# Kernel optimization log

Measured on AMD Instinct MI355X. Metric: run time of the kernel, lower is better.

The kernel has to match this reference:

```python
import jax, jax.numpy as jnp
import numpy as np

B, C, W = 32, 128, 4096          # batch, channel (= emb_dim = D), window/input_dim
HID = [2048, 1024, 512]          # encoder hidden dims (last dim transforms)
K, D = 512, 128                  # codebook: K = hidden_dims[-1], D = emb_dim
BETA = 0.25


def setup_inputs() -> dict:
    key = jax.random.key(0)
    ks = jax.random.split(key, 12)
    def lin(k, fan_in, fan_out):
        return jax.random.normal(k, (fan_in, fan_out), jnp.float32) * (1.0 / np.sqrt(fan_in))
    inp = {"x": jax.random.normal(ks[0], (B, C, W), jnp.float32)}
    edims = [W] + HID  # 4096 -> 2048 -> 1024 -> 512
    for i in range(3):
        inp[f"ew{i}"] = lin(ks[1 + i], edims[i], edims[i + 1])
        inp[f"eb{i}"] = jnp.zeros((edims[i + 1],), jnp.float32)
    inp["codebook"] = jax.random.uniform(ks[4], (K, D), jnp.float32, -1.0 / K, 1.0 / K)
    ddims = [512, 1024, 2048, 4096]  # decoder mirrors encoder
    for i in range(3):
        inp[f"dw{i}"] = lin(ks[5 + i], ddims[i], ddims[i + 1])
        inp[f"db{i}"] = jnp.zeros((ddims[i + 1],), jnp.float32)
    return inp


def reference(x, ew0, eb0, ew1, eb1, ew2, eb2, codebook, dw0, db0, dw1, db1, dw2, db2):
    # ---- encoder: LinearBlock = Linear + ReLU over last dim ----
    h = x
    for wgt, b in ((ew0, eb0), (ew1, eb1), (ew2, eb2)):
        h = jax.nn.relu(h @ wgt + b)            # [B, C, L] with L shrinking to 512

    # ---- VectorQuantizer1d ----
    lat = jnp.swapaxes(h, 1, 2)                 # [B, L, D]
    flat = lat.reshape(-1, D)                   # [B*L, D]
    # cdist^2 via expansion, then argmin -> nearest-codebook lookup
    dist = (jnp.sum(flat * flat, axis=1, keepdims=True)
            + jnp.sum(codebook * codebook, axis=1)
            - 2.0 * flat @ codebook.T)          # [B*L, K]
    inds = jnp.argmin(dist, axis=1)             # [B*L]
    q = codebook[inds].reshape(lat.shape)       # one-hot matmul == gather

    commit = jnp.mean((jax.lax.stop_gradient(q) - lat) ** 2)
    embed = jnp.mean((q - jax.lax.stop_gradient(lat)) ** 2)
    vq_loss = BETA * commit + embed

    q_st = lat + jax.lax.stop_gradient(q - lat)  # straight-through estimator
    z = jnp.swapaxes(q_st, 1, 2)                 # back to [B, D, L]

    # ---- decoder: Linear+ReLU blocks, last block has no activation ----
    for i, (wgt, b) in enumerate(((dw0, db0), (dw1, db1), (dw2, db2))):
        z = z @ wgt + b
        if i < 2:
            z = jax.nn.relu(z)
    return z, x, vq_loss
```

## Files before the change

### kernel.cpp

```cpp
#include <hip/hip_runtime.h>


typedef _Float16 f16;
typedef _Float16 f16x8 __attribute__((ext_vector_type(8)));
typedef _Float16 f16x4 __attribute__((ext_vector_type(4)));
typedef float    f32x4 __attribute__((ext_vector_type(4)));

typedef const unsigned int __attribute__((address_space(1)))* gp1_t;
typedef unsigned int __attribute__((address_space(3)))*       lp3_t;

__device__ __forceinline__ void gl_lds16(const void* g, void* l) {
  __builtin_amdgcn_global_load_lds((gp1_t)g, (lp3_t)l, 16, 0, 0);
}

#define BATCH 32
#define CDIM  128
#define WDIM  4096
#define LDIM  512
#define KCB   512
#define DCB   128

#define SX    128.0f
#define SW    256.0f
#define SA    256.0f
#define SCB   4096.0f
#define SQ    4096.0f

#define G8_BAR() do { asm volatile("" ::: "memory"); \
  __builtin_amdgcn_s_barrier(); asm volatile("" ::: "memory"); } while (0)
#define G8_LGKM0() do { asm volatile("s_waitcnt lgkmcnt(0)" ::: "memory"); \
  __builtin_amdgcn_sched_barrier(0); } while (0)
#define G8_PRIO1() __builtin_amdgcn_s_setprio(1)
#define G8_PRIO0() __builtin_amdgcn_s_setprio(0)


#define GS_STAGE(src, row0, kk, off) \
  _Pragma("unroll") \
  for (int j_ = 0; j_ < 2; ++j_) { \
    const int p_ = j_ * 8192 + tid * 16; \
    const int r_ = p_ >> 6; \
    const int c_ = (p_ >> 4) & 3; \
    gl_lds16((src) + (size_t)((row0) + r_) * K + (kk) + ((c_ ^ ((r_ >> 1) & 3)) << 3), \
             smem + (off) + p_); \
  }

#define GS_ST(tt, pb, SRC, row0, poff) do { \
  const int tc_ = (tt) < NTloc ? (tt) : NTloc - 1; \
  const int kk_ = (t0 + tc_) << 5; \
  GS_STAGE(SRC, row0, kk_, (pb) * 65536 + (poff)) } while (0)

#define GS_READ_A(pb, HL, half, dst) \
  _Pragma("unroll") \
  for (int m_ = 0; m_ < 4; ++m_) { \
    const int r_ = wr * 128 + ((half) * 4 + m_) * 16 + fr; \
    dst[m_] = *(const f16x8*)(smem + (pb) * 65536 + (HL) * 16384 + r_ * 64 + swz16); \
  }

#define GS_READ_B(pb, HL, brr) \
  _Pragma("unroll") \
  for (int n_ = 0; n_ < 4; ++n_) { \
    const int r_ = wc * 64 + n_ * 16 + fr; \
    brr[n_] = *(const f16x8*)(smem + (pb) * 65536 + 32768 + (HL) * 16384 + r_ * 64 + swz16); \
  }

#define GS_MFMA(aarr, half, brr) \
  _Pragma("unroll") \
  for (int m_ = 0; m_ < 4; ++m_) \
  _Pragma("unroll") \
  for (int n_ = 0; n_ < 4; ++n_) \
    acc[(half) * 4 + m_][n_] = __builtin_amdgcn_mfma_f32_16x16x32_f16( \
        aarr[m_], brr[n_], acc[(half) * 4 + m_][n_], 0, 0, 0);

__global__ __launch_bounds__(512, 2)
void vq_gemmS(const f16* __restrict__ Ah, const f16* __restrict__ Al,
              const f16* __restrict__ Bh, const f16* __restrict__ Bl,
              float* __restrict__ Co, int M, int N, int K, int NTloc)
{
  __shared__ __align__(16) char smem[131072];

  const int tid = threadIdx.x;
  const int lane = tid & 63;
  const int w = tid >> 6;
  const int wr = w >> 2, wc = w & 3;
  const int fr = lane & 15, hq = lane >> 4;
  const int swz16 = (hq ^ ((fr >> 1) & 3)) << 4;

  const int nbx = N / 256;
  const int cpx = (int)gridDim.x >> 3;
  const int swzb = ((int)blockIdx.x & 7) * cpx + ((int)blockIdx.x >> 3);
  const int bx = swzb % nbx, by = swzb / nbx;
  const int m0 = by * 256, n0 = bx * 256;
  const int t0 = (int)blockIdx.y * NTloc;

  f32x4 acc[8][4] = {};
  f16x8 ah0[4], ah1[4], al0[4], al1[4], bh[4], bl[4];

  GS_ST(0, 0, Bh, n0, 32768); GS_ST(0, 0, Bl, n0, 49152);
  GS_ST(0, 0, Ah, m0, 0);     GS_ST(0, 0, Al, m0, 16384);
  GS_ST(1, 1, Bh, n0, 32768); GS_ST(1, 1, Bl, n0, 49152);
  GS_ST(1, 1, Ah, m0, 0);     GS_ST(1, 1, Al, m0, 16384);

  int pb = 0;
  for (int t = 0; t < NTloc; ++t) {
    asm volatile("s_waitcnt vmcnt(8)" ::: "memory");
    G8_BAR();
    GS_READ_A(pb, 0, 0, ah0) GS_READ_B(pb, 0, bh)
    G8_BAR(); G8_LGKM0();
    G8_PRIO1(); GS_MFMA(ah0, 0, bh) G8_PRIO0();
    G8_BAR();
    GS_READ_A(pb, 1, 0, al0) GS_READ_B(pb, 1, bl)
    GS_ST(t + 2, pb, Bh, n0, 32768);
    G8_BAR(); G8_LGKM0();
    G8_PRIO1(); GS_MFMA(ah0, 0, bl) G8_PRIO0();
    G8_BAR();
    GS_READ_A(pb, 0, 1, ah1)
    GS_ST(t + 2, pb, Bl, n0, 49152);
    G8_BAR(); G8_LGKM0();
    G8_PRIO1(); GS_MFMA(al0, 0, bh) G8_PRIO0();
    G8_BAR();
    GS_READ_A(pb, 1, 1, al1)
    GS_ST(t + 2, pb, Ah, m0, 0);
    G8_BAR(); G8_LGKM0();
    G8_PRIO1(); GS_MFMA(ah1, 1, bh) G8_PRIO0();
    G8_BAR();
    GS_ST(t + 2, pb, Al, m0, 16384);
    G8_PRIO1(); GS_MFMA(ah1, 1, bl) GS_MFMA(al1, 1, bh) G8_PRIO0();
    pb ^= 1;
  }

  float* Pslab = Co + (size_t)blockIdx.y * M * N;
  const int r4 = hq * 4;
#pragma unroll
  for (int mi = 0; mi < 8; ++mi) {
#pragma unroll
    for (int ni = 0; ni < 4; ++ni) {
      const int col = n0 + wc * 64 + ni * 16 + fr;
#pragma unroll
      for (int j = 0; j < 4; ++j) {
        const int row = m0 + wr * 128 + mi * 16 + r4 + j;
        Pslab[(size_t)row * N + col] = acc[mi][ni][j];
      }
    }
  }
}


#define G8_SRC(t, As, Bs, kk) \
  const f16 *As, *Bs; int kk; \
  { int ts_ = (t) < NTloc ? (t) : NTloc - 1; int kg_ = (t0 + ts_) << 6; \
    if (SPLIT) { int sg_ = (kg_ >= 2 * K) ? 2 : ((kg_ >= K) ? 1 : 0); \
      kk = kg_ - sg_ * K; As = (sg_ == 2) ? Al : Ah; Bs = (sg_ == 1) ? Bl : Bh; } \
    else { As = Ah; Bs = Bh; kk = kg_; } }

#define G8_STAGE(src, row0, kk, off) \
  _Pragma("unroll") \
  for (int j_ = 0; j_ < 2; ++j_) { \
    const int p_ = j_ * 8192 + tid * 16; \
    const int r_ = p_ >> 7; \
    const int c_ = (p_ >> 4) & 7; \
    gl_lds16((src) + (size_t)((row0) + r_) * K + (kk) + ((c_ ^ (r_ & 7)) << 3), \
             smem + (off) + p_); \
  }

#define G8_STAGE_A(t, u) do { G8_SRC(t, As_, Bs_, kk_) \
  G8_STAGE(As_, m0 + (u) * 128, kk_, ((t) & 1) * ASZ + (u) * 16384) } while (0)
#define G8_STAGE_B(t, u) do { G8_SRC(t, As_, Bs_, kk_) \
  G8_STAGE(Bs_, n0 + (u) * 128, kk_, BBASE + ((t) & 1) * BSZ + (u) * 16384) } while (0)

#define G8_READ_A(buf, mh) \
  _Pragma("unroll") \
  for (int m_ = 0; m_ < MR2; ++m_) { \
    const int r_ = wr * (MR * 16) + ((mh) * MR2 + m_) * 16 + fr; \
    _Pragma("unroll") \
    for (int ks_ = 0; ks_ < 2; ++ks_) \
      ar[m_][ks_] = *(const f16x8*)(smem + (buf) * ASZ + r_ * 128 + \
                                    ((((ks_ << 2) + hq) ^ (r_ & 7)) << 4)); \
  }

#define G8_READ_B(buf, nh, br) \
  _Pragma("unroll") \
  for (int n_ = 0; n_ < 2; ++n_) { \
    const int r_ = wc * 64 + ((nh) * 2 + n_) * 16 + fr; \
    _Pragma("unroll") \
    for (int ks_ = 0; ks_ < 2; ++ks_) \
      br[n_][ks_] = *(const f16x8*)(smem + BBASE + (buf) * BSZ + r_ * 128 + \
                                    ((((ks_ << 2) + hq) ^ (r_ & 7)) << 4)); \
  }

#define G8_MFMA(mh, nh, br) \
  _Pragma("unroll") \
  for (int m_ = 0; m_ < MR2; ++m_) \
  _Pragma("unroll") \
  for (int n_ = 0; n_ < 2; ++n_) \
  _Pragma("unroll") \
  for (int ks_ = 0; ks_ < 2; ++ks_) \
    acc[(mh) * MR2 + m_][(nh) * 2 + n_] = __builtin_amdgcn_mfma_f32_16x16x32_f16( \
        ar[m_][ks_], br[n_][ks_], acc[(mh) * MR2 + m_][(nh) * 2 + n_], 0, 0, 0);

#define G8_VMGATE() do { \
  if constexpr (BUNITS == 2) asm volatile("s_waitcnt vmcnt(4)" ::: "memory"); \
  else                       asm volatile("s_waitcnt vmcnt(2)" ::: "memory"); } while (0)

template<int SPLIT, int EPI, int WM, int WN, int MR>
__global__ __launch_bounds__(512, 2)
void vq_gemm8(const f16* __restrict__ Ah, const f16* __restrict__ Al,
              const f16* __restrict__ Bh, const f16* __restrict__ Bl,
              const float* __restrict__ bias,
              void* __restrict__ Co, void* __restrict__ Co2,
              int M, int N, int K, int NTloc, float unscale, float outscale)
{
  constexpr int MR2 = MR / 2;
  constexpr int GBM = WM * MR * 16;
  constexpr int GBN = WN * 64;
  constexpr int BUNITS = GBN / 128;
  constexpr int ASZ = GBM * 128;
  constexpr int BSZ = GBN * 128;
  constexpr int BBASE = 2 * ASZ;
  constexpr int LDSZ = 2 * ASZ + 2 * BSZ;

  __shared__ __align__(16) char smem[LDSZ];

  const int tid = threadIdx.x;
  const int lane = tid & 63;
  const int w = tid >> 6;
  const int wr = w / WN, wc = w % WN;
  const int fr = lane & 15, hq = lane >> 4;

  const int nbx = N / GBN;
  const int cpx = (int)gridDim.x >> 3;
  const int swz = ((int)blockIdx.x & 7) * cpx + ((int)blockIdx.x >> 3);
  const int bx = swz % nbx, by = swz / nbx;
  const int m0 = by * GBM, n0 = bx * GBN;
  const int t0 = (int)blockIdx.y * NTloc;

  const int NI = NTloc >> 1;

  f32x4 acc[MR][4] = {};
  f16x8 ar[MR2][2], br0[2][2], br1[2][2];

  G8_STAGE_B(0, 0); if constexpr (BUNITS == 2) G8_STAGE_B(0, 1);
  G8_STAGE_A(0, 0); G8_STAGE_A(0, 1);
  G8_STAGE_B(1, 0); if constexpr (BUNITS == 2) G8_STAGE_B(1, 1);

  for (int i = 0; i < NI; ++i) {
    const int to = 2 * i + 1, te = 2 * i + 2, to2 = 2 * i + 3;
    if constexpr (BUNITS == 1) {
      G8_VMGATE(); G8_BAR();
      G8_READ_A(0, 0) G8_READ_B(0, 0, br0) G8_READ_B(0, 1, br1)
      G8_STAGE_A(to, 0); G8_STAGE_A(to, 1);
      G8_BAR(); G8_LGKM0();
      G8_PRIO1(); G8_MFMA(0, 0, br0) G8_MFMA(0, 1, br1) G8_PRIO0();
      G8_BAR();
      G8_READ_A(0, 1)
      G8_STAGE_B(te, 0);
      G8_BAR(); G8_LGKM0();
      G8_PRIO1(); G8_MFMA(1, 0, br0) G8_MFMA(1, 1, br1) G8_PRIO0();
      G8_VMGATE(); G8_BAR();
      G8_READ_A(1, 0) G8_READ_B(1, 0, br0) G8_READ_B(1, 1, br1)
      G8_STAGE_A(te, 0); G8_STAGE_A(te, 1);
      G8_BAR(); G8_LGKM0();
      G8_PRIO1(); G8_MFMA(0, 0, br0) G8_MFMA(0, 1, br1) G8_PRIO0();
      G8_BAR();
      G8_READ_A(1, 1)
      G8_STAGE_B(to2, 0);
      G8_BAR(); G8_LGKM0();
      G8_PRIO1(); G8_MFMA(1, 0, br0) G8_MFMA(1, 1, br1) G8_PRIO0();
    } else {
      G8_VMGATE(); G8_BAR();
      G8_READ_A(0, 0) G8_READ_B(0, 0, br0)
      G8_STAGE_A(to, 0);
      G8_BAR(); G8_LGKM0(); G8_PRIO1(); G8_MFMA(0, 0, br0) G8_PRIO0();
      G8_BAR();
      G8_READ_B(0, 1, br1)
      G8_STAGE_A(to, 1);
      G8_BAR(); G8_LGKM0(); G8_PRIO1(); G8_MFMA(0, 1, br1) G8_PRIO0();
      G8_BAR();
      G8_READ_A(0, 1)
      G8_STAGE_B(te, 0);
      G8_BAR(); G8_LGKM0(); G8_PRIO1(); G8_MFMA(1, 0, br0) G8_PRIO0();
      G8_BAR();
      G8_STAGE_B(te, 1);
      G8_BAR(); G8_PRIO1(); G8_MFMA(1, 1, br1) G8_PRIO0();
      G8_VMGATE(); G8_BAR();
      G8_READ_A(1, 0) G8_READ_B(1, 0, br0)
      G8_STAGE_A(te, 0);
      G8_BAR(); G8_LGKM0(); G8_PRIO1(); G8_MFMA(0, 0, br0) G8_PRIO0();
      G8_BAR();
      G8_READ_B(1, 1, br1)
      G8_STAGE_A(te, 1);
      G8_BAR(); G8_LGKM0(); G8_PRIO1(); G8_MFMA(0, 1, br1) G8_PRIO0();
      G8_BAR();
      G8_READ_A(1, 1)
      G8_STAGE_B(to2, 0);
      G8_BAR(); G8_LGKM0(); G8_PRIO1(); G8_MFMA(1, 0, br0) G8_PRIO0();
      G8_BAR();
      G8_STAGE_B(to2, 1);
      G8_BAR(); G8_PRIO1(); G8_MFMA(1, 1, br1) G8_PRIO0();
    }
  }

  const int r4 = hq * 4;
#pragma unroll
  for (int mi = 0; mi < MR; ++mi) {
#pragma unroll
    for (int ni = 0; ni < 4; ++ni) {
      const int col = n0 + wc * 64 + ni * 16 + fr;
      const float bv = (EPI == 0) ? 0.f : bias[col];
#pragma unroll
      for (int j = 0; j < 4; ++j) {
        const int row = m0 + wr * (MR * 16) + mi * 16 + r4 + j;
        const size_t idx = (size_t)row * N + col;
        float y = acc[mi][ni][j] * unscale;
        if (EPI != 0) y += bv;
        if (EPI == 1 || EPI == 2) y = fmaxf(y, 0.f);
        if (EPI == 0 || EPI == 3) ((float*)Co)[idx] = y;
        else {
          const float ys = y * outscale;
          const f16 hv = (f16)ys;
          ((f16*)Co)[idx] = hv;
          if (EPI == 1) ((f16*)Co2)[idx] = (f16)(ys - (float)hv);
        }
      }
    }
  }
}

template<int NS>
__global__ void vq_ksum(const float* __restrict__ P, const float* __restrict__ bias,
                        f16* __restrict__ Oh, f16* __restrict__ Ol,
                        int MN, int N, float unscale, float outscale)
{
  const int i4 = (blockIdx.x * 256 + threadIdx.x) * 4;
  if (i4 >= MN) return;
  float4 s = ((const float4*)P)[i4 >> 2];
#pragma unroll
  for (int sl = 1; sl < NS; ++sl) {
    const float4 v = ((const float4*)(P + (size_t)sl * MN))[i4 >> 2];
    s.x += v.x; s.y += v.y; s.z += v.z; s.w += v.w;
  }
  const int col = i4 % N;
  f16x4 h, l;
#pragma unroll
  for (int j = 0; j < 4; ++j) {
    float y = (&s.x)[j] * unscale + bias[col + j];
    y = fmaxf(y, 0.f) * outscale;
    const f16 hv = (f16)y;
    h[j] = hv;
    l[j] = (f16)(y - (float)hv);
  }
  *(f16x4*)&Oh[i4] = h;
  *(f16x4*)&Ol[i4] = l;
}

#define BM 128
#define BN 128
#define BK 32

template<int SPLIT, int EPI>
__global__ __launch_bounds__(256, 2)
void vq_gemm(const f16* __restrict__ Ah, const f16* __restrict__ Al,
             const f16* __restrict__ Bh, const f16* __restrict__ Bl,
             const float* __restrict__ bias,
             void* __restrict__ Co, void* __restrict__ Co2,
             int M, int N, int K, float unscale, float outscale)
{
  __shared__ __align__(16) f16 sAh[BM * BK];
  __shared__ __align__(16) f16 sBh[BN * BK];
  __shared__ __align__(16) f16 sAl[SPLIT ? BM * BK : 8];
  __shared__ __align__(16) f16 sBl[SPLIT ? BN * BK : 8];

  const int tid  = threadIdx.x;
  const int lane = tid & 63;
  const int w    = tid >> 6;
  const int nb   = N / BN;
  const int bx   = blockIdx.x % nb;
  const int by   = blockIdx.x / nb;
  const int m0   = by * BM, n0 = bx * BN;
  const int wr   = w >> 1, wc = w & 1;
  const int fr   = lane & 15;
  const int ko   = (lane >> 4) * 8;

  f32x4 acc[4][4] = {};

  const int srow = lane >> 2;
  const int skb  = (lane & 3) * 8;

  for (int k0 = 0; k0 < K; k0 += BK) {
#pragma unroll
    for (int i = 0; i < 2; ++i) {
      const int c  = w * 2 + i;
      const size_t ga = (size_t)(m0 + c * 16 + srow) * K + k0 + skb;
      const size_t gb = (size_t)(n0 + c * 16 + srow) * K + k0 + skb;
      gl_lds16(Ah + ga, &sAh[c * 512]);
      gl_lds16(Bh + gb, &sBh[c * 512]);
      if (SPLIT) {
        gl_lds16(Al + ga, &sAl[c * 512]);
        gl_lds16(Bl + gb, &sBl[c * 512]);
      }
    }
    __syncthreads();

    f16x8 ah[4], bh[4], al[4], bl[4];
#pragma unroll
    for (int mi = 0; mi < 4; ++mi) {
      const int r = (wr * 64 + mi * 16 + fr) * BK + ko;
      ah[mi] = *(const f16x8*)&sAh[r];
      if (SPLIT) al[mi] = *(const f16x8*)&sAl[r];
    }
#pragma unroll
    for (int ni = 0; ni < 4; ++ni) {
      const int r = (wc * 64 + ni * 16 + fr) * BK + ko;
      bh[ni] = *(const f16x8*)&sBh[r];
      if (SPLIT) bl[ni] = *(const f16x8*)&sBl[r];
    }
#pragma unroll
    for (int mi = 0; mi < 4; ++mi)
#pragma unroll
      for (int ni = 0; ni < 4; ++ni) {
        acc[mi][ni] = __builtin_amdgcn_mfma_f32_16x16x32_f16(ah[mi], bh[ni], acc[mi][ni], 0, 0, 0);
        if (SPLIT) {
          acc[mi][ni] = __builtin_amdgcn_mfma_f32_16x16x32_f16(ah[mi], bl[ni], acc[mi][ni], 0, 0, 0);
          acc[mi][ni] = __builtin_amdgcn_mfma_f32_16x16x32_f16(al[mi], bh[ni], acc[mi][ni], 0, 0, 0);
        }
      }
    __syncthreads();
  }

  const int r4 = (lane >> 4) * 4;
#pragma unroll
  for (int mi = 0; mi < 4; ++mi) {
#pragma unroll
    for (int ni = 0; ni < 4; ++ni) {
      const int col = n0 + wc * 64 + ni * 16 + fr;
      const float bv = (EPI == 0) ? 0.0f : bias[col];
#pragma unroll
      for (int j = 0; j < 4; ++j) {
        const int row = m0 + wr * 64 + mi * 16 + r4 + j;
        float y = acc[mi][ni][j] * unscale;
        if (EPI != 0) y += bv;
        if (EPI == 1 || EPI == 2) y = fmaxf(y, 0.0f);
        const size_t idx = (size_t)row * N + col;
        if (EPI == 0 || EPI == 3) {
          ((float*)Co)[idx] = y;
        } else {
          const float ys = y * outscale;
          const f16 hv = (f16)ys;
          ((f16*)Co)[idx] = hv;
          if (EPI == 1) ((f16*)Co2)[idx] = (f16)(ys - (float)hv);
        }
      }
    }
  }
}

__global__ void vq_prep(const float* __restrict__ x, f16* __restrict__ XH,
                        f16* __restrict__ XL, float* __restrict__ raw,
                        const float* __restrict__ cb, f16* __restrict__ CBH,
                        f16* __restrict__ CBL, float* __restrict__ cbn)
{
  const int b = blockIdx.x;
  if (b < 16384) {
    const int i = b * 256 + threadIdx.x;
    const float4 v = ((const float4*)x)[i];
    ((float4*)raw)[i] = v;
    f16x4 h, l;
#pragma unroll
    for (int j = 0; j < 4; ++j) {
      const float s = (&v.x)[j] * SX;
      const f16 hh = (f16)s;
      h[j] = hh;
      l[j] = (f16)(s - (float)hh);
    }
    *(f16x4*)&XH[i * 4] = h;
    *(f16x4*)&XL[i * 4] = l;
  } else if (b < 16448) {
    const int i = (b - 16384) * 256 + threadIdx.x;
    const float4 v = ((const float4*)cb)[i];
    f16x4 h, l;
#pragma unroll
    for (int j = 0; j < 4; ++j) {
      const float s = (&v.x)[j] * SCB;
      const f16 hh = (f16)s;
      h[j] = hh;
      l[j] = (f16)(s - (float)hh);
    }
    *(f16x4*)&CBH[i * 4] = h;
    *(f16x4*)&CBL[i * 4] = l;
  } else {
    const int k = (b - 16448) * 256 + threadIdx.x;
    if (k < KCB) {
      float s = 0.f;
      for (int c = 0; c < DCB; ++c) { const float v = cb[k * DCB + c]; s += v * v; }
      cbn[k] = s;
    }
  }
}

__global__ void vq_tsplit_all(
    const float* __restrict__ ew0, f16* __restrict__ EW0H, f16* __restrict__ EW0L,
    const float* __restrict__ ew1, f16* __restrict__ EW1H, f16* __restrict__ EW1L,
    const float* __restrict__ ew2, f16* __restrict__ EW2H, f16* __restrict__ EW2L,
    const float* __restrict__ dw0, f16* __restrict__ DW0,
    const float* __restrict__ dw1, f16* __restrict__ DW1,
    const float* __restrict__ dw2, f16* __restrict__ DW2)
{
  __shared__ float t[32][33];
  int b = blockIdx.x;
  const float* W; f16* Th; f16* Tl; int K, N, gx, wl;
  if (b < 8192)        { W = ew0; Th = EW0H; Tl = EW0L; K = 4096; N = 2048; gx = 64;  wl = 1; }
  else if (b < 10240)  { b -= 8192;  W = ew1; Th = EW1H; Tl = EW1L; K = 2048; N = 1024; gx = 32;  wl = 1; }
  else if (b < 10752)  { b -= 10240; W = ew2; Th = EW2H; Tl = EW2L; K = 1024; N = 512;  gx = 16;  wl = 1; }
  else if (b < 11264)  { b -= 10752; W = dw0; Th = DW0;  Tl = nullptr; K = 512;  N = 1024; gx = 32;  wl = 0; }
  else if (b < 13312)  { b -= 11264; W = dw1; Th = DW1;  Tl = nullptr; K = 1024; N = 2048; gx = 64;  wl = 0; }
  else                 { b -= 13312; W = dw2; Th = DW2;  Tl = nullptr; K = 2048; N = 4096; gx = 128; wl = 0; }
  const int n0 = (b % gx) * 32, k0 = (b / gx) * 32;
  const int tx = threadIdx.x & 31, ty = threadIdx.x >> 5;
#pragma unroll
  for (int i = 0; i < 4; ++i)
    t[ty + i * 8][tx] = W[(size_t)(k0 + ty + i * 8) * N + n0 + tx];
  __syncthreads();
#pragma unroll
  for (int i = 0; i < 4; ++i) {
    const int n = n0 + ty + i * 8;
    const float v = t[tx][ty + i * 8] * SW;
    const f16 hv = (f16)v;
    Th[(size_t)n * K + k0 + tx] = hv;
    if (wl) Tl[(size_t)n * K + k0 + tx] = (f16)(v - (float)hv);
  }
}

__global__ void vq_tpose(const f16* __restrict__ Hh, const f16* __restrict__ Hl,
                         f16* __restrict__ Fh, f16* __restrict__ Fl)
{
  __shared__ f16 th[32][33];
  __shared__ f16 tl[32][33];
  const int bidx = blockIdx.x;
  const int b = bidx >> 6, rem = bidx & 63;
  const int l0 = (rem >> 2) * 32, c0 = (rem & 3) * 32;
  const int tx = threadIdx.x & 31, ty = threadIdx.x >> 5;
  const size_t hbase = (size_t)b * CDIM * LDIM;
#pragma unroll
  for (int i = 0; i < 4; ++i) {
    const int c = c0 + ty + i * 8;
    th[ty + i * 8][tx] = Hh[hbase + (size_t)c * LDIM + l0 + tx];
    tl[ty + i * 8][tx] = Hl[hbase + (size_t)c * LDIM + l0 + tx];
  }
  __syncthreads();
  const size_t fbase = (size_t)b * LDIM * DCB;
#pragma unroll
  for (int i = 0; i < 4; ++i) {
    const int l = l0 + ty + i * 8;
    Fh[fbase + (size_t)l * DCB + c0 + tx] = th[tx][ty + i * 8];
    Fl[fbase + (size_t)l * DCB + c0 + tx] = tl[tx][ty + i * 8];
  }
}

__global__ void vq_argmin(const float* __restrict__ G, const float* __restrict__ cbn,
                          int* __restrict__ inds)
{
  const int row = blockIdx.x;
  const int lane = threadIdx.x;
  const float* g = G + (size_t)row * KCB;
  float best = 1e30f; int bi = 0;
#pragma unroll
  for (int j = 0; j < 8; ++j) {
    const int k = j * 64 + lane;
    const float d = cbn[k] - 2.0f * g[k];
    if (d < best) { best = d; bi = k; }
  }
  for (int off = 32; off; off >>= 1) {
    const float ov = __shfl_xor(best, off);
    const int oi = __shfl_xor(bi, off);
    if (ov < best || (ov == best && oi < bi)) { best = ov; bi = oi; }
  }
  if (lane == 0) inds[row] = bi;
}

__global__ void vq_gather_loss(const float* __restrict__ cb, const int* __restrict__ inds,
                               f16* __restrict__ z0,
                               const f16* __restrict__ Fh, const f16* __restrict__ Fl,
                               float* __restrict__ partials)
{
  if (blockIdx.x < 8192) {
    const int t = blockIdx.x * 256 + threadIdx.x;
    const int l = t & 511, c = (t >> 9) & 127, b = t >> 16;
    const int ind = inds[b * LDIM + l];
    z0[t] = (f16)(cb[ind * DCB + c] * SQ);
  } else {
    const int bid = blockIdx.x - 8192;
    const int gw = (bid * 256 + threadIdx.x) >> 6;
    const int lane = threadIdx.x & 63;
    float s = 0.f;
    for (int r = gw; r < BATCH * LDIM; r += 1024) {
      const int ind = inds[r];
      const f16* fh = Fh + (size_t)r * DCB;
      const f16* fl = Fl + (size_t)r * DCB;
      const float* q = cb + (size_t)ind * DCB;
#pragma unroll
      for (int j = 0; j < 2; ++j) {
        const int c = j * 64 + lane;
        const float lat = ((float)fh[c] + (float)fl[c]) * (1.0f / SA);
        const float d = q[c] - lat;
        s += d * d;
      }
    }
    for (int off = 32; off; off >>= 1) s += __shfl_xor(s, off);
    __shared__ float wsum[4];
    if (lane == 0) wsum[threadIdx.x >> 6] = s;
    __syncthreads();
    if (threadIdx.x == 0) partials[bid] = wsum[0] + wsum[1] + wsum[2] + wsum[3];
  }
}

__global__ void vq_loss_final(const float* __restrict__ partials, float* __restrict__ out)
{
  float s = partials[threadIdx.x];
  for (int off = 32; off; off >>= 1) s += __shfl_xor(s, off);
  __shared__ float wsum[4];
  if ((threadIdx.x & 63) == 0) wsum[threadIdx.x >> 6] = s;
  __syncthreads();
  if (threadIdx.x == 0)
    out[0] = (wsum[0] + wsum[1] + wsum[2] + wsum[3]) * (1.25f / (float)(BATCH * LDIM * DCB));
}

extern "C" void kernel_launch(void* const* d_in, const int* in_sizes, int n_in,
                              void* d_out, int out_size, void* d_ws, size_t ws_size,
                              hipStream_t stream)
{
  const float* x   = (const float*)d_in[0];
  const float* ew0 = (const float*)d_in[1];
  const float* eb0 = (const float*)d_in[2];
  const float* ew1 = (const float*)d_in[3];
  const float* eb1 = (const float*)d_in[4];
  const float* ew2 = (const float*)d_in[5];
  const float* eb2 = (const float*)d_in[6];
  const float* cb  = (const float*)d_in[7];
  const float* dw0 = (const float*)d_in[8];
  const float* db0 = (const float*)d_in[9];
  const float* dw1 = (const float*)d_in[10];
  const float* db1 = (const float*)d_in[11];
  const float* dw2 = (const float*)d_in[12];
  const float* db2 = (const float*)d_in[13];
  float* out = (float*)d_out;

  constexpr size_t N_X  = 4096ull * 4096;
  constexpr size_t N_E0 = 4096ull * 2048, N_E1 = 2048ull * 1024, N_E2 = 1024ull * 512;
  constexpr size_t N_CB = 512ull * 128;
  constexpr size_t N_D0 = 512ull * 1024, N_D1 = 1024ull * 2048, N_D2 = 2048ull * 4096;
  constexpr size_t N_H0 = 4096ull * 2048, N_H1 = 4096ull * 1024, N_H2 = 4096ull * 512;
  constexpr size_t N_FL = 16384ull * 128;
  constexpr size_t N_Z1 = 4096ull * 1024;

  constexpr size_t O_EW0H = 0;
  constexpr size_t O_EW0L = O_EW0H + N_E0 * 2;
  constexpr size_t O_EW1H = O_EW0L + N_E0 * 2;
  constexpr size_t O_EW1L = O_EW1H + N_E1 * 2;
  constexpr size_t O_EW2H = O_EW1L + N_E1 * 2;
  constexpr size_t O_EW2L = O_EW2H + N_E2 * 2;
  constexpr size_t O_CBH  = O_EW2L + N_E2 * 2;
  constexpr size_t O_CBL  = O_CBH + N_CB * 2;
  constexpr size_t O_DW0  = O_CBL + N_CB * 2;
  constexpr size_t O_DW1  = O_DW0 + N_D0 * 2;
  constexpr size_t O_DW2  = O_DW1 + N_D1 * 2;
  constexpr size_t O_XH   = O_DW2 + N_D2 * 2;
  constexpr size_t O_XL   = O_XH + N_X * 2;
  constexpr size_t O_H0H  = O_XL + N_X * 2;
  constexpr size_t O_H0L  = O_H0H + N_H0 * 2;
  constexpr size_t O_H1H  = O_H0L + N_H0 * 2;
  constexpr size_t O_H1L  = O_H1H + N_H1 * 2;
  constexpr size_t O_H2H  = O_H1L + N_H1 * 2;
  constexpr size_t O_H2L  = O_H2H + N_H2 * 2;
  constexpr size_t O_FLH  = O_H2L + N_H2 * 2;
  constexpr size_t O_FLL  = O_FLH + N_FL * 2;
  constexpr size_t O_G    = O_XH;
  constexpr size_t O_INDS = O_XL;
  constexpr size_t O_CBN  = O_XL + (1ull << 17);
  constexpr size_t O_PART = O_XL + (1ull << 18);
  constexpr size_t O_Z0   = O_XL + (1ull << 20);
  constexpr size_t O_ZH1  = O_Z0 + N_H2 * 2;
  constexpr size_t O_ZH2  = O_ZH1 + N_Z1 * 2;

  char* ws = (char*)d_ws;
  f16*   XH = (f16*)(ws + O_XH);   f16* XL = (f16*)(ws + O_XL);
  f16* EW0H = (f16*)(ws + O_EW0H); f16* EW0L = (f16*)(ws + O_EW0L);
  f16* EW1H = (f16*)(ws + O_EW1H); f16* EW1L = (f16*)(ws + O_EW1L);
  f16* EW2H = (f16*)(ws + O_EW2H); f16* EW2L = (f16*)(ws + O_EW2L);
  f16*  CBH = (f16*)(ws + O_CBH);  f16* CBL = (f16*)(ws + O_CBL);
  f16*  DW0 = (f16*)(ws + O_DW0);  f16* DW1 = (f16*)(ws + O_DW1);  f16* DW2 = (f16*)(ws + O_DW2);
  f16*  H0H = (f16*)(ws + O_H0H);  f16* H0L = (f16*)(ws + O_H0L);
  f16*  H1H = (f16*)(ws + O_H1H);  f16* H1L = (f16*)(ws + O_H1L);
  f16*  H2H = (f16*)(ws + O_H2H);  f16* H2L = (f16*)(ws + O_H2L);
  f16*  FLH = (f16*)(ws + O_FLH);  f16* FLL = (f16*)(ws + O_FLL);
  float*  G = (float*)(ws + O_G);
  int* INDS = (int*)(ws + O_INDS);
  float* CBN = (float*)(ws + O_CBN);
  float* PART = (float*)(ws + O_PART);
  f16*   Z0 = (f16*)(ws + O_Z0);
  f16*  ZH1 = (f16*)(ws + O_ZH1);
  f16*  ZH2 = (f16*)(ws + O_ZH2);
  float* PSL = out;

  vq_prep<<<16450, 256, 0, stream>>>(x, XH, XL, out + 16777216, cb, CBH, CBL, CBN);
  vq_tsplit_all<<<21504, 256, 0, stream>>>(ew0, EW0H, EW0L, ew1, EW1H, EW1L,
                                           ew2, EW2H, EW2L, dw0, DW0, dw1, DW1, dw2, DW2);

  vq_gemmS<<<dim3(128, 2), 512, 0, stream>>>(
      XH, XL, EW0H, EW0L, PSL, 4096, 2048, 4096, 64);
  vq_ksum<2><<<(int)(N_H0 / 4 / 256), 256, 0, stream>>>(
      PSL, eb0, H0H, H0L, (int)N_H0, 2048, 1.0f / (SX * SW), SA);
  vq_gemmS<<<dim3(64, 4), 512, 0, stream>>>(
      H0H, H0L, EW1H, EW1L, PSL, 4096, 1024, 2048, 16);
  vq_ksum<4><<<(int)(N_H1 / 4 / 256), 256, 0, stream>>>(
      PSL, eb1, H1H, H1L, (int)N_H1, 1024, 1.0f / (SA * SW), SA);
  vq_gemm<1, 1><<<(4096 / BM) * (512 / BN), 256, 0, stream>>>(
      H1H, H1L, EW2H, EW2L, eb2, H2H, H2L, 4096, 512, 1024, 1.0f / (SA * SW), SA);

  vq_tpose<<<BATCH * 64, 256, 0, stream>>>(H2H, H2L, FLH, FLL);
  vq_gemm<1, 0><<<(16384 / BM) * (512 / BN), 256, 0, stream>>>(
      FLH, FLL, CBH, CBL, nullptr, G, nullptr, 16384, 512, 128, 1.0f / (SA * SCB), 0.f);
  vq_argmin<<<16384, 64, 0, stream>>>(G, CBN, INDS);
  vq_gather_loss<<<8448, 256, 0, stream>>>(cb, INDS, Z0, FLH, FLL, PART);
  vq_loss_final<<<1, 256, 0, stream>>>(PART, out + 33554432);

  vq_gemm<0, 2><<<(4096 / BM) * (1024 / BN), 256, 0, stream>>>(
      Z0, nullptr, DW0, nullptr, db0, ZH1, nullptr, 4096, 1024, 512, 1.0f / (SQ * SW), SQ);
  vq_gemm8<0, 2, 4, 2, 4><<<dim3(256, 1), 512, 0, stream>>>(
      ZH1, nullptr, DW1, nullptr, db1, ZH2, nullptr, 4096, 2048, 1024, 16, 1.0f / (SQ * SW), SQ);
  vq_gemm8<0, 3, 2, 4, 8><<<dim3(256, 1), 512, 0, stream>>>(
      ZH2, nullptr, DW2, nullptr, db2, out, nullptr, 4096, 4096, 2048, 32, 1.0f / (SQ * SW), 0.f);

  (void)in_sizes; (void)n_in; (void)out_size; (void)ws_size;
}
```

Measured before the change: 513.4 us.

## Fuse codebook distance argmin into the VQ GEMM epilogue

The codebook distance GEMM now reduces each 128-column tile to a per-row best (value, index) candidate inside its epilogue, using shuffles and shared memory, instead of writing the full 16384x512 fp32 distance matrix. A small kernel then merges the four column-tile candidates per row. This removes the large G write and re-read and the one-row-per-block argmin launch. In exchange it adds shared-memory reductions and a sync to the GEMM epilogue, and it relies on the block index decomposition (bx) matching four column tiles.

```diff
diff --git a/kernel.cpp b/kernel.cpp
--- a/kernel.cpp
+++ b/kernel.cpp
@@ -427,6 +427,46 @@
   }
 
   const int r4 = (lane >> 4) * 4;
+
+  if constexpr (EPI == 5) {
+    __shared__ float cv[2][128];
+    __shared__ int   ci[2][128];
+#pragma unroll
+    for (int mi = 0; mi < 4; ++mi) {
+#pragma unroll
+      for (int j = 0; j < 4; ++j) {
+        float best = 1e30f; int bi = 0;
+#pragma unroll
+        for (int ni = 0; ni < 4; ++ni) {
+          const int colL = wc * 64 + ni * 16 + fr;
+          const float d = bias[n0 + colL] - 2.0f * (acc[mi][ni][j] * unscale);
+          if (d < best || (d == best && colL < bi)) { best = d; bi = colL; }
+        }
+#pragma unroll
+        for (int off = 8; off; off >>= 1) {
+          const float ov = __shfl_xor(best, off);
+          const int oi = __shfl_xor(bi, off);
+          if (ov < best || (ov == best && oi < bi)) { best = ov; bi = oi; }
+        }
+        if (fr == 0) {
+          const int lr = wr * 64 + mi * 16 + r4 + j;
+          cv[wc][lr] = best; ci[wc][lr] = bi;
+        }
+      }
+    }
+    __syncthreads();
+    if (tid < 128) {
+      const float v0 = cv[0][tid], v1 = cv[1][tid];
+      const int i0 = ci[0][tid], i1 = ci[1][tid];
+      float v; int ii;
+      if (v1 < v0 || (v1 == v0 && i1 < i0)) { v = v1; ii = i1; }
+      else                                  { v = v0; ii = i0; }
+      ((float*)Co)[(size_t)(m0 + tid) * 4 + bx] = v;
+      ((int*)Co2)[(size_t)(m0 + tid) * 4 + bx] = ii + n0;
+    }
+    return;
+  }
+
 #pragma unroll
   for (int mi = 0; mi < 4; ++mi) {
 #pragma unroll
@@ -453,6 +493,21 @@
   }
 }
 
+__global__ void vq_argmin4(const float* __restrict__ CV, const int* __restrict__ CI,
+                           int* __restrict__ inds)
+{
+  const int r = blockIdx.x * 256 + threadIdx.x;
+  if (r >= BATCH * LDIM) return;
+  float best = CV[(size_t)r * 4]; int bi = CI[(size_t)r * 4];
+#pragma unroll
+  for (int b = 1; b < 4; ++b) {
+    const float v = CV[(size_t)r * 4 + b];
+    const int i = CI[(size_t)r * 4 + b];
+    if (v < best || (v == best && i < bi)) { best = v; bi = i; }
+  }
+  inds[r] = bi;
+}
+
 __global__ void vq_prep(const float* __restrict__ x, f16* __restrict__ XH,
                         f16* __restrict__ XL, float* __restrict__ raw,
                         const float* __restrict__ cb, f16* __restrict__ CBH,
@@ -553,27 +608,6 @@
     Fh[fbase + (size_t)l * DCB + c0 + tx] = th[tx][ty + i * 8];
     Fl[fbase + (size_t)l * DCB + c0 + tx] = tl[tx][ty + i * 8];
   }
-}
-
-__global__ void vq_argmin(const float* __restrict__ G, const float* __restrict__ cbn,
-                          int* __restrict__ inds)
-{
-  const int row = blockIdx.x;
-  const int lane = threadIdx.x;
-  const float* g = G + (size_t)row * KCB;
-  float best = 1e30f; int bi = 0;
-#pragma unroll
-  for (int j = 0; j < 8; ++j) {
-    const int k = j * 64 + lane;
-    const float d = cbn[k] - 2.0f * g[k];
-    if (d < best) { best = d; bi = k; }
-  }
-  for (int off = 32; off; off >>= 1) {
-    const float ov = __shfl_xor(best, off);
-    const int oi = __shfl_xor(bi, off);
-    if (ov < best || (ov == best && oi < bi)) { best = ov; bi = oi; }
-  }
-  if (lane == 0) inds[row] = bi;
 }
 
 __global__ void vq_gather_loss(const float* __restrict__ cb, const int* __restrict__ inds,
@@ -672,7 +706,8 @@
   constexpr size_t O_H2L  = O_H2H + N_H2 * 2;
   constexpr size_t O_FLH  = O_H2L + N_H2 * 2;
   constexpr size_t O_FLL  = O_FLH + N_FL * 2;
-  constexpr size_t O_G    = O_XH;
+  constexpr size_t O_CANDV = O_XH;
+  constexpr size_t O_CANDI = O_XH + (1ull << 18);
   constexpr size_t O_INDS = O_XL;
   constexpr size_t O_CBN  = O_XL + (1ull << 17);
   constexpr size_t O_PART = O_XL + (1ull << 18);
@@ -691,7 +726,8 @@
   f16*  H1H = (f16*)(ws + O_H1H);  f16* H1L = (f16*)(ws + O_H1L);
   f16*  H2H = (f16*)(ws + O_H2H);  f16* H2L = (f16*)(ws + O_H2L);
   f16*  FLH = (f16*)(ws + O_FLH);  f16* FLL = (f16*)(ws + O_FLL);
-  float*  G = (float*)(ws + O_G);
+  float* CANDV = (float*)(ws + O_CANDV);
+  int*   CANDI = (int*)(ws + O_CANDI);
   int* INDS = (int*)(ws + O_INDS);
   float* CBN = (float*)(ws + O_CBN);
   float* PART = (float*)(ws + O_PART);
@@ -716,9 +752,9 @@
       H1H, H1L, EW2H, EW2L, eb2, H2H, H2L, 4096, 512, 1024, 1.0f / (SA * SW), SA);
 
   vq_tpose<<<BATCH * 64, 256, 0, stream>>>(H2H, H2L, FLH, FLL);
-  vq_gemm<1, 0><<<(16384 / BM) * (512 / BN), 256, 0, stream>>>(
-      FLH, FLL, CBH, CBL, nullptr, G, nullptr, 16384, 512, 128, 1.0f / (SA * SCB), 0.f);
-  vq_argmin<<<16384, 64, 0, stream>>>(G, CBN, INDS);
+  vq_gemm<1, 5><<<(16384 / BM) * (512 / BN), 256, 0, stream>>>(
+      FLH, FLL, CBH, CBL, CBN, CANDV, CANDI, 16384, 512, 128, 1.0f / (SA * SCB), 0.f);
+  vq_argmin4<<<(BATCH * LDIM) / 256, 256, 0, stream>>>(CANDV, CANDI, INDS);
   vq_gather_loss<<<8448, 256, 0, stream>>>(cb, INDS, Z0, FLH, FLL, PART);
   vq_loss_final<<<1, 256, 0, stream>>>(PART, out + 33554432);
 
```

Result: no change. 506.9 us (-1.3%).
